# Kernel optimization log

Hardware: AMD Instinct MI355X
Metric: run time of the kernel (lower is better)

## Reference

```python
import jax, jax.numpy as jnp
import numpy as np


def setup_inputs() -> dict:
    key = jax.random.key(0)
    ks = jax.random.split(key, 8)
    C = 256
    x = jax.random.normal(ks[0], (8, C, 64, 64), dtype=jnp.float32)
    scale = 1.0 / np.sqrt(C)
    Wb = jax.random.normal(ks[1], (C, C), dtype=jnp.float32) * scale
    bb = jax.random.normal(ks[2], (C,), dtype=jnp.float32) * 0.01
    Wc = jax.random.normal(ks[3], (C, C), dtype=jnp.float32) * scale
    bc = jax.random.normal(ks[4], (C,), dtype=jnp.float32) * 0.01
    Wd = jax.random.normal(ks[5], (C, C), dtype=jnp.float32) * scale
    bd = jax.random.normal(ks[6], (C,), dtype=jnp.float32) * 0.01
    alpha = jnp.zeros((1,), dtype=jnp.float32) + 0.1  # nonzero so output depends on attention path
    return {"x": x, "Wb": Wb, "bb": bb, "Wc": Wc, "bc": bc, "Wd": Wd, "bd": bd, "alpha": alpha}


def _pam(x, Wb, bb, Wc, bc, Wd, bd, alpha):
    n, c, h, w = x.shape
    xf = x.reshape(n, c, h * w)  # [n, c, N]
    # 1x1 conv == per-pixel linear over channels: W @ x + b
    B = jnp.einsum('oc,ncl->nlo', Wb, xf) + bb  # [n, N, c]
    Cm = jnp.einsum('oc,ncl->nol', Wc, xf) + bc[None, :, None]  # [n, c, N]
    D = jnp.einsum('oc,ncl->nlo', Wd, xf) + bd  # [n, N, c]
    attn = jax.nn.softmax(jnp.einsum('nic,ncj->nij', B, Cm), axis=-1)  # [n, N, N]
    y = jnp.einsum('nij,njc->nic', attn, D)  # [n, N, c]
    y = y.transpose(0, 2, 1).reshape(n, c, h, w)
    return alpha * y + x


def reference(x, Wb, bb, Wc, bc, Wd, bd, alpha):
    return _pam(x, Wb, bb, Wc, bc, Wd, bd, alpha)
```

## Files before the change

### kernel.cpp

```cpp
#include <hip/hip_runtime.h>

using bf16x8 = __attribute__((ext_vector_type(8))) short;
using f32x4  = __attribute__((ext_vector_type(4))) float;
using f32x16 = __attribute__((ext_vector_type(16))) float;
using u32x4  = __attribute__((ext_vector_type(4))) unsigned int;

#define NPIX 4096
#define CCH  256

__device__ __forceinline__ unsigned short f2bf(float f) {
  unsigned int u = __builtin_bit_cast(unsigned int, f);
  u += 0x7FFFu + ((u >> 16) & 1u);
  return (unsigned short)(u >> 16);
}

__device__ __forceinline__ float bfu(unsigned short h) {
  unsigned int u = ((unsigned int)h) << 16;
  return __builtin_bit_cast(float, u);
}

__device__ __forceinline__ unsigned int pack2(float a, float b) {
  return (unsigned int)f2bf(a) | ((unsigned int)f2bf(b) << 16);
}

__device__ __forceinline__ void gld_lds16(const void* g, void* l) {
  __builtin_amdgcn_global_load_lds(
      (const __attribute__((address_space(1))) unsigned int*)g,
      (__attribute__((address_space(3))) unsigned int*)l, 16, 0, 0);
}

__global__ __launch_bounds__(256) void convert_w_kernel(
    const float* __restrict__ Wb, const float* __restrict__ Wc,
    const float* __restrict__ Wd, unsigned short* __restrict__ Wbf) {
  const int mat = blockIdx.y;
  const float* src = (mat == 0) ? Wb : (mat == 1) ? Wc : Wd;
  int i = (blockIdx.x * 256 + threadIdx.x) * 4;
  float4 v = *reinterpret_cast<const float4*>(src + i);
  uint2 o;
  o.x = pack2(v.x, v.y);
  o.y = pack2(v.z, v.w);
  *reinterpret_cast<uint2*>(Wbf + mat * 65536 + i) = o;
}

__global__ __launch_bounds__(256, 2) void fused_proj_kernel(
    const float* __restrict__ x, const unsigned short* __restrict__ Wbf,
    const float* __restrict__ bb, const float* __restrict__ bc,
    const float* __restrict__ bd, unsigned short* __restrict__ Q,
    unsigned short* __restrict__ K, unsigned short* __restrict__ Vt) {
  __shared__ __align__(16) float tile[64][65];
  __shared__ __align__(16) char xsub[32768];
  char* bounce = (char*)tile;

  const int tid = threadIdx.x;
  const int wid = tid >> 6, lane = tid & 63;
  const int l31 = lane & 31, hi = lane >> 5;
  const int lt = blockIdx.x, n = blockIdx.y;

  #pragma unroll 1
  for (int ct = 0; ct < 4; ++ct) {
    const float* xg = x + ((size_t)(n * CCH + ct * 64)) * NPIX + lt * 64;
    #pragma unroll
    for (int it = 0; it < 4; ++it) {
      int row = (tid >> 4) + it * 16;
      int col = (tid & 15) * 4;
      float4 v = *reinterpret_cast<const float4*>(xg + (size_t)row * NPIX + col);
      tile[row][col] = v.x; tile[row][col + 1] = v.y;
      tile[row][col + 2] = v.z; tile[row][col + 3] = v.w;
    }
    __syncthreads();
    #pragma unroll
    for (int it = 0; it < 2; ++it) {
      int idx = tid + it * 256;
      int l = idx >> 3;
      int ch = (idx & 7) * 8;
      int c = ct * 64 + ch;
      uint4 o;
      o.x = pack2(tile[ch + 0][l], tile[ch + 1][l]);
      o.y = pack2(tile[ch + 2][l], tile[ch + 3][l]);
      o.z = pack2(tile[ch + 4][l], tile[ch + 5][l]);
      o.w = pack2(tile[ch + 6][l], tile[ch + 7][l]);
      int addr = (l >> 5) * 16384 + (c >> 4) * 1024 + ((c >> 3) & 1) * 512 + (l & 31) * 16;
      *reinterpret_cast<uint4*>(xsub + addr) = o;
    }
    __syncthreads();
  }

  const int o0a = wid * 64, o0b = wid * 64 + 32;
  const size_t pixrow = (size_t)n * NPIX + lt * 64;

  #pragma unroll 1
  for (int mat = 0; mat < 3; ++mat) {
    const unsigned short* W = Wbf + mat * 65536;
    const float* bias = (mat == 0) ? bb : (mat == 1) ? bc : bd;
    f32x16 a00, a01, a10, a11;
    #pragma unroll
    for (int e = 0; e < 16; ++e) { a00[e] = 0.f; a01[e] = 0.f; a10[e] = 0.f; a11[e] = 0.f; }
    #pragma unroll
    for (int c0 = 0; c0 < 16; ++c0) {
      bf16x8 x0 = *reinterpret_cast<const bf16x8*>(xsub + c0 * 1024 + lane * 16);
      bf16x8 x1 = *reinterpret_cast<const bf16x8*>(xsub + 16384 + c0 * 1024 + lane * 16);
      bf16x8 w0 = *reinterpret_cast<const bf16x8*>(W + (o0a + l31) * CCH + c0 * 16 + hi * 8);
      bf16x8 w1 = *reinterpret_cast<const bf16x8*>(W + (o0b + l31) * CCH + c0 * 16 + hi * 8);
      if (mat < 2) {
        a00 = __builtin_amdgcn_mfma_f32_32x32x16_bf16(w0, x0, a00, 0, 0, 0);
        a01 = __builtin_amdgcn_mfma_f32_32x32x16_bf16(w0, x1, a01, 0, 0, 0);
        a10 = __builtin_amdgcn_mfma_f32_32x32x16_bf16(w1, x0, a10, 0, 0, 0);
        a11 = __builtin_amdgcn_mfma_f32_32x32x16_bf16(w1, x1, a11, 0, 0, 0);
      } else {
        a00 = __builtin_amdgcn_mfma_f32_32x32x16_bf16(x0, w0, a00, 0, 0, 0);
        a01 = __builtin_amdgcn_mfma_f32_32x32x16_bf16(x1, w0, a01, 0, 0, 0);
        a10 = __builtin_amdgcn_mfma_f32_32x32x16_bf16(x0, w1, a10, 0, 0, 0);
        a11 = __builtin_amdgcn_mfma_f32_32x32x16_bf16(x1, w1, a11, 0, 0, 0);
      }
    }
    if (mat < 2) {
      unsigned short* dst = (mat == 0) ? Q : K;
      #pragma unroll 1
      for (int ph = 0; ph < 2; ++ph) {
        __syncthreads();
        const f32x16& A0 = ph ? a01 : a00;
        const f32x16& A1 = ph ? a11 : a10;
        const int swz = (l31 & 15) << 4;
        #pragma unroll
        for (int r2 = 0; r2 < 8; ++r2) {
          const int r = r2 * 2;
          const int od = (r & 3) + 8 * (r >> 2) + 4 * hi;
          const int oa = o0a + od, ob = o0b + od;
          *reinterpret_cast<unsigned int*>(bounce + ((l31 * 512 + oa * 2) ^ swz)) =
              pack2(A0[r] + bias[oa], A0[r + 1] + bias[oa + 1]);
          *reinterpret_cast<unsigned int*>(bounce + ((l31 * 512 + ob * 2) ^ swz)) =
              pack2(A1[r] + bias[ob], A1[r + 1] + bias[ob + 1]);
        }
        __syncthreads();
        const int dp = tid >> 3, obase = (tid & 7) * 32;
        const int dswz = (dp & 15) << 4;
        char* gout = (char*)(dst + (pixrow + ph * 32 + dp) * CCH + obase);
        #pragma unroll
        for (int k = 0; k < 4; ++k) {
          u32x4 v = *reinterpret_cast<const u32x4*>(
              bounce + ((dp * 512 + obase * 2 + k * 16) ^ dswz));
          *reinterpret_cast<u32x4*>(gout + k * 16) = v;
        }
      }
    } else {
      #pragma unroll 1
      for (int os = 0; os < 2; ++os) {
        __syncthreads();
        if ((wid >> 1) == os) {
          const int ola = o0a + l31 - os * 128, olb = o0b + l31 - os * 128;
          const float bva = bias[o0a + l31], bvb = bias[o0b + l31];
          const int sza = (ola & 7) << 4, szb = (olb & 7) << 4;
          #pragma unroll
          for (int r2 = 0; r2 < 8; ++r2) {
            const int r = r2 * 2;
            const int pd = (r & 3) + 8 * (r >> 2) + 4 * hi;
            *reinterpret_cast<unsigned int*>(bounce + ((ola * 128 + pd * 2) ^ sza)) =
                pack2(a00[r] + bva, a00[r + 1] + bva);
            *reinterpret_cast<unsigned int*>(bounce + ((ola * 128 + (pd + 32) * 2) ^ sza)) =
                pack2(a01[r] + bva, a01[r + 1] + bva);
            *reinterpret_cast<unsigned int*>(bounce + ((olb * 128 + pd * 2) ^ szb)) =
                pack2(a10[r] + bvb, a10[r + 1] + bvb);
            *reinterpret_cast<unsigned int*>(bounce + ((olb * 128 + (pd + 32) * 2) ^ szb)) =
                pack2(a11[r] + bvb, a11[r + 1] + bvb);
          }
        }
        __syncthreads();
        const int ol = tid >> 1, pb0 = (tid & 1) * 32;
        const int vswz = (ol & 7) << 4;
        char* gout = (char*)(Vt + ((size_t)(n * CCH + os * 128 + ol)) * NPIX + lt * 64 + pb0);
        #pragma unroll
        for (int k = 0; k < 4; ++k) {
          u32x4 v = *reinterpret_cast<const u32x4*>(
              bounce + ((ol * 128 + pb0 * 2 + k * 16) ^ vswz));
          *reinterpret_cast<u32x4*>(gout + k * 16) = v;
        }
      }
    }
  }
}

__global__ __launch_bounds__(256, 2) void attn_part_kernel(
    const unsigned short* __restrict__ Q, const unsigned short* __restrict__ K,
    const unsigned short* __restrict__ Vt, unsigned short* __restrict__ Opart,
    float* __restrict__ lsumbuf) {
  __shared__ __align__(16) char smem[65536];

  const int tid = threadIdx.x;
  const int wid = tid >> 6;
  const int lane = tid & 63;
  const int l31 = lane & 31;
  const int hi = lane >> 5;
  const int lofs = lane << 4;
  const int blk = blockIdx.x;
  const int n = blk & 7;
  const int t2 = blk >> 3;
  const int half = t2 & 1;
  const int qb = t2 >> 1;
  const int q0 = qb * 128 + wid * 32;

  const unsigned short* Qg = Q + (size_t)n * NPIX * CCH;
  const char* Kg = (const char*)(K + ((size_t)n * NPIX + half * 2048) * CCH);
  const char* Vg = (const char*)(Vt + (size_t)n * CCH * NPIX + half * 2048);

  bf16x8 qf[16];
  #pragma unroll
  for (int c0 = 0; c0 < 16; ++c0)
    qf[c0] = *reinterpret_cast<const bf16x8*>(
        Qg + (size_t)(q0 + l31) * CCH + c0 * 16 + hi * 8);

  f32x16 oacc[8];
  #pragma unroll
  for (int i = 0; i < 8; ++i)
    #pragma unroll
    for (int e = 0; e < 16; ++e) oacc[i][e] = 0.f;
  float lsum = 0.f;

  int soffK[4], soffV[4];
  #pragma unroll
  for (int g = 0; g < 4; ++g) {
    const int s = wid * 4 + g;
    soffK[g] = l31 * 512 + s * 32 + hi * 16;
    const int cb = s >> 1, kk2 = s & 1;
    soffV[g] = (cb * 32 + l31) * 8192 + (kk2 * 16 + hi * 8) * 2;
  }

  auto STAGE_K = [&](int par_, int adv) {
    #pragma unroll
    for (int g = 0; g < 4; ++g)
      gld_lds16(Kg + (size_t)soffK[g] + (size_t)adv,
                smem + par_ * 32768 + (wid * 4 + g) * 1024);
  };
  auto STAGE_V = [&](int par_, int adv) {
    #pragma unroll
    for (int g = 0; g < 4; ++g)
      gld_lds16(Vg + (size_t)soffV[g] + (size_t)adv,
                smem + par_ * 32768 + 16384 + (wid * 4 + g) * 1024);
  };

  STAGE_K(0, 0);
  STAGE_V(0, 0);

  #pragma unroll 1
  for (int t = 0; t < 64; ++t) {
    const int par = t & 1;
    const char* kb = smem + par * 32768;
    const char* vb = kb + 16384;
    const int tn = (t + 1) & 63;

    STAGE_K(par ^ 1, tn * 16384);
    __builtin_amdgcn_sched_barrier(0);
    asm volatile("s_waitcnt vmcnt(8)" ::: "memory");
    __builtin_amdgcn_s_barrier();
    __builtin_amdgcn_sched_barrier(0);

    f32x16 S;
    #pragma unroll
    for (int e = 0; e < 16; ++e) S[e] = 0.f;
    __builtin_amdgcn_s_setprio(1);
    #pragma unroll
    for (int c0 = 0; c0 < 16; ++c0) {
      bf16x8 kf = *reinterpret_cast<const bf16x8*>(kb + c0 * 1024 + lofs);
      S = __builtin_amdgcn_mfma_f32_32x32x16_bf16(kf, qf[c0], S, 0, 0, 0);
    }
    __builtin_amdgcn_s_setprio(0);

    STAGE_V(par ^ 1, tn * 64);

    float rsum = 0.f;
    unsigned int pw[8];
    #pragma unroll
    for (int i = 0; i < 8; ++i) {
      float p0 = exp2f(fmaf(S[2 * i],     1.44269504f, -101.0f));
      float p1 = exp2f(fmaf(S[2 * i + 1], 1.44269504f, -101.0f));
      rsum += p0 + p1;
      unsigned int r;
      asm("v_cvt_pk_bf16_f32 %0, %1, %2" : "=v"(r) : "v"(p0), "v"(p1));
      pw[i] = r;
    }
    lsum += rsum;

    unsigned int s0a = pw[0], s0b = pw[2];
    unsigned int s1a = pw[1], s1b = pw[3];
    unsigned int s2a = pw[4], s2b = pw[6];
    unsigned int s3a = pw[5], s3b = pw[7];
    asm volatile("v_permlane32_swap_b32 %0, %1" : "+v"(s0a), "+v"(s0b));
    asm volatile("v_permlane32_swap_b32 %0, %1" : "+v"(s1a), "+v"(s1b));
    asm volatile("v_permlane32_swap_b32 %0, %1" : "+v"(s2a), "+v"(s2b));
    asm volatile("v_permlane32_swap_b32 %0, %1" : "+v"(s3a), "+v"(s3b));
    u32x4 f0, f1;
    f0[0] = s0a; f0[1] = s1a; f0[2] = s0b; f0[3] = s1b;
    f1[0] = s2a; f1[1] = s3a; f1[2] = s2b; f1[3] = s3b;
    bf16x8 pa0 = __builtin_bit_cast(bf16x8, f0);
    bf16x8 pa1 = __builtin_bit_cast(bf16x8, f1);

    __builtin_amdgcn_sched_barrier(0);
    asm volatile("s_waitcnt vmcnt(8)" ::: "memory");
    __builtin_amdgcn_s_barrier();
    __builtin_amdgcn_sched_barrier(0);

    __builtin_amdgcn_s_setprio(1);
    #pragma unroll
    for (int cb = 0; cb < 8; ++cb) {
      bf16x8 v0 = *reinterpret_cast<const bf16x8*>(vb + (cb * 2 + 0) * 1024 + lofs);
      oacc[cb] = __builtin_amdgcn_mfma_f32_32x32x16_bf16(pa0, v0, oacc[cb], 0, 0, 0);
      bf16x8 v1 = *reinterpret_cast<const bf16x8*>(vb + (cb * 2 + 1) * 1024 + lofs);
      oacc[cb] = __builtin_amdgcn_mfma_f32_32x32x16_bf16(pa1, v1, oacc[cb], 0, 0, 0);
    }
    __builtin_amdgcn_s_setprio(0);
  }

  asm volatile("s_waitcnt vmcnt(0)" ::: "memory");

  lsum += __shfl_xor(lsum, 32);
  char* slab = (char*)Opart + (size_t)blk * 65536;
  #pragma unroll
  for (int cb = 0; cb < 8; ++cb) {
    u32x4 u0, u1;
    u0[0] = pack2(oacc[cb][0],  oacc[cb][1]);
    u0[1] = pack2(oacc[cb][2],  oacc[cb][3]);
    u0[2] = pack2(oacc[cb][4],  oacc[cb][5]);
    u0[3] = pack2(oacc[cb][6],  oacc[cb][7]);
    u1[0] = pack2(oacc[cb][8],  oacc[cb][9]);
    u1[1] = pack2(oacc[cb][10], oacc[cb][11]);
    u1[2] = pack2(oacc[cb][12], oacc[cb][13]);
    u1[3] = pack2(oacc[cb][14], oacc[cb][15]);
    *reinterpret_cast<u32x4*>(slab + (cb * 2 + 0) * 4096 + tid * 16) = u0;
    *reinterpret_cast<u32x4*>(slab + (cb * 2 + 1) * 4096 + tid * 16) = u1;
  }
  if (hi == 0) lsumbuf[blk * 128 + wid * 32 + l31] = lsum;
}

__global__ __launch_bounds__(512) void merge_kernel(
    const unsigned short* __restrict__ Opart, const float* __restrict__ lsumbuf,
    const float* __restrict__ x, const float* __restrict__ alpha_p,
    float* __restrict__ out) {
  __shared__ float T[32768];
  __shared__ float Lq[128];

  const int tid = threadIdx.x;
  const int pr8 = tid >> 6;
  const int lane = tid & 63;
  const int l31 = lane & 31;
  const int hi = lane >> 5;
  const int qsub = pr8 & 3;
  const int cbh = pr8 >> 2;
  const int atid = qsub * 64 + lane;
  const int m = blockIdx.x;
  const int n = m & 7;
  const int qb = m >> 3;
  const int blkA = n + 8 * (0 + 2 * qb);
  const int blkB = n + 8 * (1 + 2 * qb);

  if (tid < 128)
    Lq[tid] = alpha_p[0] / (lsumbuf[blkA * 128 + tid] + lsumbuf[blkB * 128 + tid]);
  __syncthreads();

  const char* sa = (const char*)Opart + (size_t)blkA * 65536;
  const char* sb = (const char*)Opart + (size_t)blkB * 65536;

  #pragma unroll
  for (int cbi = 0; cbi < 4; ++cbi) {
    const int cb = cbh * 4 + cbi;
    const int c = cb * 32 + l31;
    const int swz = c & 28;
    #pragma unroll
    for (int h = 0; h < 2; ++h) {
      u32x4 a = *reinterpret_cast<const u32x4*>(sa + (cb * 2 + h) * 4096 + atid * 16);
      u32x4 b = *reinterpret_cast<const u32x4*>(sb + (cb * 2 + h) * 4096 + atid * 16);
      #pragma unroll
      for (int w = 0; w < 4; ++w) {
        const int r = h * 8 + w * 2;
        float v0 = bfu((unsigned short)(a[w] & 0xFFFF)) + bfu((unsigned short)(b[w] & 0xFFFF));
        float v1 = bfu((unsigned short)(a[w] >> 16)) + bfu((unsigned short)(b[w] >> 16));
        const int q0l = qsub * 32 + ((r) & 3) + 8 * ((r) >> 2) + 4 * hi;
        const int q1l = q0l + 1;
        T[c * 128 + (q0l ^ swz)] = v0 * Lq[q0l];
        T[c * 128 + (q1l ^ swz)] = v1 * Lq[q1l];
      }
    }
  }
  __syncthreads();

  const int l0 = (tid & 31) * 4;
  #pragma unroll 4
  for (int sw = 0; sw < 16; ++sw) {
    const int c = (tid >> 5) + sw * 16;
    const float* src = &T[c * 128 + (l0 ^ (c & 28))];
    float4 v = *reinterpret_cast<const float4*>(src);
    const size_t g = ((size_t)n * CCH + c) * NPIX + qb * 128 + l0;
    float4 xi = *reinterpret_cast<const float4*>(x + g);
    float4 o;
    o.x = v.x + xi.x; o.y = v.y + xi.y; o.z = v.z + xi.z; o.w = v.w + xi.w;
    *reinterpret_cast<float4*>(out + g) = o;
  }
}

extern "C" void kernel_launch(void* const* d_in, const int* in_sizes, int n_in,
                              void* d_out, int out_size, void* d_ws, size_t ws_size,
                              hipStream_t stream) {
  const float* x  = (const float*)d_in[0];
  const float* Wb = (const float*)d_in[1];
  const float* bb = (const float*)d_in[2];
  const float* Wc = (const float*)d_in[3];
  const float* bc = (const float*)d_in[4];
  const float* Wd = (const float*)d_in[5];
  const float* bd = (const float*)d_in[6];
  const float* alpha = (const float*)d_in[7];
  float* out = (float*)d_out;
  char* ws = (char*)d_ws;

  unsigned short* Wbf   = (unsigned short*)(ws);
  unsigned short* Q     = (unsigned short*)(ws + 393216);
  unsigned short* K     = (unsigned short*)(ws + 17170432);
  unsigned short* Vt    = (unsigned short*)(ws + 33947648);
  unsigned short* Opart = (unsigned short*)(ws + 50724864);
  float*          lsumb = (float*)(ws + 84279296);

  convert_w_kernel<<<dim3(64, 3), 256, 0, stream>>>(Wb, Wc, Wd, Wbf);
  fused_proj_kernel<<<dim3(64, 8), 256, 0, stream>>>(x, Wbf, bb, bc, bd, Q, K, Vt);
  attn_part_kernel<<<dim3(512), 256, 0, stream>>>(Q, K, Vt, Opart, lsumb);
  merge_kernel<<<dim3(256), 512, 0, stream>>>(Opart, lsumb, x, alpha, out);
}
```

Measured before the change: 218.9 us.

## Software-pipeline attention loop so softmax of tile t overlaps PV MFMA of tile t-1

Restructures the flash-attention main loop into a prologue, a steady state and an epilogue. In each iteration the QK MFMAs for tile t run, then the exp/convert softmax work for tile t is interleaved with the PV MFMAs for tile t-1 using the previous P fragments. K and V get separate double buffers, with K prefetched two tiles ahead. This is meant to hide the VALU exp latency behind matrix work and remove one barrier per iteration, at the cost of more live registers for the carried P fragments and more complex vmcnt accounting.

```diff
diff --git a/kernel.cpp b/kernel.cpp
--- a/kernel.cpp
+++ b/kernel.cpp
@@ -215,44 +215,40 @@
     for (int e = 0; e < 16; ++e) oacc[i][e] = 0.f;
   float lsum = 0.f;
 
-  int soffK[4], soffV[4];
+  int soffK[4];
   #pragma unroll
-  for (int g = 0; g < 4; ++g) {
-    const int s = wid * 4 + g;
-    soffK[g] = l31 * 512 + s * 32 + hi * 16;
-    const int cb = s >> 1, kk2 = s & 1;
-    soffV[g] = (cb * 32 + l31) * 8192 + (kk2 * 16 + hi * 8) * 2;
-  }
-
-  auto STAGE_K = [&](int par_, int adv) {
+  for (int g = 0; g < 4; ++g)
+    soffK[g] = l31 * 512 + (wid * 4 + g) * 32 + hi * 16;
+
+  auto STAGE_K = [&](int par_, int tt) {
     #pragma unroll
     for (int g = 0; g < 4; ++g)
-      gld_lds16(Kg + (size_t)soffK[g] + (size_t)adv,
-                smem + par_ * 32768 + (wid * 4 + g) * 1024);
+      gld_lds16(Kg + (size_t)soffK[g] + (size_t)tt * 16384,
+                smem + par_ * 16384 + (wid * 4 + g) * 1024);
   };
-  auto STAGE_V = [&](int par_, int adv) {
-    #pragma unroll
-    for (int g = 0; g < 4; ++g)
-      gld_lds16(Vg + (size_t)soffV[g] + (size_t)adv,
-                smem + par_ * 32768 + 16384 + (wid * 4 + g) * 1024);
+  auto STAGE_V = [&](int par_, int tt) {
+    #pragma unroll
+    for (int g = 0; g < 4; ++g) {
+      const int s = wid * 4 + g;
+      const int cb = s >> 1, kk2 = s & 1;
+      const int off = (cb * 32 + l31) * 8192 + (kk2 * 16 + hi * 8) * 2;
+      gld_lds16(Vg + (size_t)off + (size_t)tt * 64,
+                smem + 32768 + par_ * 16384 + (wid * 4 + g) * 1024);
+    }
   };
 
+  bf16x8 pa0p, pa1p;
+
   STAGE_K(0, 0);
+  STAGE_K(1, 1);
   STAGE_V(0, 0);
-
-  #pragma unroll 1
-  for (int t = 0; t < 64; ++t) {
-    const int par = t & 1;
-    const char* kb = smem + par * 32768;
-    const char* vb = kb + 16384;
-    const int tn = (t + 1) & 63;
-
-    STAGE_K(par ^ 1, tn * 16384);
-    __builtin_amdgcn_sched_barrier(0);
-    asm volatile("s_waitcnt vmcnt(8)" ::: "memory");
-    __builtin_amdgcn_s_barrier();
-    __builtin_amdgcn_sched_barrier(0);
-
+  __builtin_amdgcn_sched_barrier(0);
+  asm volatile("s_waitcnt vmcnt(8)" ::: "memory");
+  __builtin_amdgcn_s_barrier();
+  __builtin_amdgcn_sched_barrier(0);
+
+  {
+    const char* kb = smem;
     f32x16 S;
     #pragma unroll
     for (int e = 0; e < 16; ++e) S[e] = 0.f;
@@ -263,8 +259,6 @@
       S = __builtin_amdgcn_mfma_f32_32x32x16_bf16(kf, qf[c0], S, 0, 0, 0);
     }
     __builtin_amdgcn_s_setprio(0);
-
-    STAGE_V(par ^ 1, tn * 64);
 
     float rsum = 0.f;
     unsigned int pw[8];
@@ -278,7 +272,6 @@
       pw[i] = r;
     }
     lsum += rsum;
-
     unsigned int s0a = pw[0], s0b = pw[2];
     unsigned int s1a = pw[1], s1b = pw[3];
     unsigned int s2a = pw[4], s2b = pw[6];
@@ -290,26 +283,83 @@
     u32x4 f0, f1;
     f0[0] = s0a; f0[1] = s1a; f0[2] = s0b; f0[3] = s1b;
     f1[0] = s2a; f1[1] = s3a; f1[2] = s2b; f1[3] = s3b;
-    bf16x8 pa0 = __builtin_bit_cast(bf16x8, f0);
-    bf16x8 pa1 = __builtin_bit_cast(bf16x8, f1);
-
+    pa0p = __builtin_bit_cast(bf16x8, f0);
+    pa1p = __builtin_bit_cast(bf16x8, f1);
+  }
+  __builtin_amdgcn_s_barrier();
+
+  #pragma unroll 1
+  for (int t = 1; t < 64; ++t) {
+    const int par = t & 1;
+    const char* kb = smem + par * 16384;
+    const char* vbp = smem + 32768 + (par ^ 1) * 16384;
+
+    STAGE_K(par ^ 1, (t + 1) & 63);
+    STAGE_V(par, t);
     __builtin_amdgcn_sched_barrier(0);
     asm volatile("s_waitcnt vmcnt(8)" ::: "memory");
     __builtin_amdgcn_s_barrier();
     __builtin_amdgcn_sched_barrier(0);
 
+    f32x16 S;
+    #pragma unroll
+    for (int e = 0; e < 16; ++e) S[e] = 0.f;
     __builtin_amdgcn_s_setprio(1);
     #pragma unroll
+    for (int c0 = 0; c0 < 16; ++c0) {
+      bf16x8 kf = *reinterpret_cast<const bf16x8*>(kb + c0 * 1024 + lofs);
+      S = __builtin_amdgcn_mfma_f32_32x32x16_bf16(kf, qf[c0], S, 0, 0, 0);
+    }
+
+    float rsum = 0.f;
+    unsigned int pw[8];
+    #pragma unroll
+    for (int i = 0; i < 8; ++i) {
+      float p0 = exp2f(fmaf(S[2 * i],     1.44269504f, -101.0f));
+      float p1 = exp2f(fmaf(S[2 * i + 1], 1.44269504f, -101.0f));
+      rsum += p0 + p1;
+      unsigned int r;
+      asm("v_cvt_pk_bf16_f32 %0, %1, %2" : "=v"(r) : "v"(p0), "v"(p1));
+      pw[i] = r;
+      bf16x8 v0 = *reinterpret_cast<const bf16x8*>(vbp + (i * 2 + 0) * 1024 + lofs);
+      oacc[i] = __builtin_amdgcn_mfma_f32_32x32x16_bf16(pa0p, v0, oacc[i], 0, 0, 0);
+      bf16x8 v1 = *reinterpret_cast<const bf16x8*>(vbp + (i * 2 + 1) * 1024 + lofs);
+      oacc[i] = __builtin_amdgcn_mfma_f32_32x32x16_bf16(pa1p, v1, oacc[i], 0, 0, 0);
+    }
+    __builtin_amdgcn_s_setprio(0);
+    lsum += rsum;
+
+    unsigned int s0a = pw[0], s0b = pw[2];
+    unsigned int s1a = pw[1], s1b = pw[3];
+    unsigned int s2a = pw[4], s2b = pw[6];
+    unsigned int s3a = pw[5], s3b = pw[7];
+    asm volatile("v_permlane32_swap_b32 %0, %1" : "+v"(s0a), "+v"(s0b));
+    asm volatile("v_permlane32_swap_b32 %0, %1" : "+v"(s1a), "+v"(s1b));
+    asm volatile("v_permlane32_swap_b32 %0, %1" : "+v"(s2a), "+v"(s2b));
+    asm volatile("v_permlane32_swap_b32 %0, %1" : "+v"(s3a), "+v"(s3b));
+    u32x4 f0, f1;
+    f0[0] = s0a; f0[1] = s1a; f0[2] = s0b; f0[3] = s1b;
+    f1[0] = s2a; f1[1] = s3a; f1[2] = s2b; f1[3] = s3b;
+    pa0p = __builtin_bit_cast(bf16x8, f0);
+    pa1p = __builtin_bit_cast(bf16x8, f1);
+
+    __builtin_amdgcn_s_barrier();
+  }
+
+  asm volatile("s_waitcnt vmcnt(0)" ::: "memory");
+  __builtin_amdgcn_s_barrier();
+  {
+    const char* vbp = smem + 32768 + 16384;
+    __builtin_amdgcn_s_setprio(1);
+    #pragma unroll
     for (int cb = 0; cb < 8; ++cb) {
-      bf16x8 v0 = *reinterpret_cast<const bf16x8*>(vb + (cb * 2 + 0) * 1024 + lofs);
-      oacc[cb] = __builtin_amdgcn_mfma_f32_32x32x16_bf16(pa0, v0, oacc[cb], 0, 0, 0);
-      bf16x8 v1 = *reinterpret_cast<const bf16x8*>(vb + (cb * 2 + 1) * 1024 + lofs);
-      oacc[cb] = __builtin_amdgcn_mfma_f32_32x32x16_bf16(pa1, v1, oacc[cb], 0, 0, 0);
+      bf16x8 v0 = *reinterpret_cast<const bf16x8*>(vbp + (cb * 2 + 0) * 1024 + lofs);
+      oacc[cb] = __builtin_amdgcn_mfma_f32_32x32x16_bf16(pa0p, v0, oacc[cb], 0, 0, 0);
+      bf16x8 v1 = *reinterpret_cast<const bf16x8*>(vbp + (cb * 2 + 1) * 1024 + lofs);
+      oacc[cb] = __builtin_amdgcn_mfma_f32_32x32x16_bf16(pa1p, v1, oacc[cb], 0, 0, 0);
     }
     __builtin_amdgcn_s_setprio(0);
   }
-
-  asm volatile("s_waitcnt vmcnt(0)" ::: "memory");
 
   lsum += __shfl_xor(lsum, 32);
   char* slab = (char*)Opart + (size_t)blk * 65536;
```

Result: no change. 217.8 us (-0.5%).
